# Performance work log

Hardware: AMD Instinct MI355X
Metric: run time of the kernel (lower is better)

## Reference

```python
import jax, jax.numpy as jnp
import numpy as np


def setup_inputs() -> dict:
    key = jax.random.key(0)
    k1, k2, k3 = jax.random.split(key, 3)
    batch, in_features, out_features = 4096, 8192, 8192
    x = jax.random.normal(k1, (batch, in_features), dtype=jnp.float32)
    weight = jax.random.normal(k2, (out_features, in_features), dtype=jnp.float32) * (1.0 / np.sqrt(in_features))
    bias = jax.random.normal(k3, (out_features,), dtype=jnp.float32) * (1.0 / np.sqrt(in_features))
    return {"x": x, "weight": weight, "bias": bias}


def reference(x, weight, bias):
    # Linear: [B, out] = x @ W^T + b
    y = jnp.einsum('bi,oi->bo', x, weight) + bias
    # Per-row sum over out_features, then mean (divide by out_features)
    mean_val = jnp.sum(y, axis=1) / weight.shape[0]  # [B]
    # Two logsumexp ops over a size-1 dim: log(exp(v)) twice == identity,
    # computed explicitly to match the original op chain.
    lse1 = jnp.log(jnp.exp(mean_val))
    lse2 = jnp.log(jnp.exp(lse1))
    return lse2[:, None]  # [B, 1]
```

## Files before the change

### kernel.cpp

```cpp
#include <hip/hip_runtime.h>

typedef float f32x4 __attribute__((ext_vector_type(4)));

constexpr int IN_F  = 8192;
constexpr int OUT_F = 8192;
constexpr int BATCH = 4096;
constexpr int TPB   = 256;
constexpr int S4    = IN_F / 4;

constexpr int CHUNKS = 256;
constexpr int RPC    = OUT_F / CHUNKS;
constexpr int COLG   = IN_F / (TPB * 4);

__global__ __launch_bounds__(TPB) void colsum_kernel(
    const float* __restrict__ W, float* __restrict__ part, int rpc) {
    const int col4 = blockIdx.x * TPB + threadIdx.x;
    const f32x4* __restrict__ p = reinterpret_cast<const f32x4*>(W)
        + (long)blockIdx.y * rpc * S4 + col4;
    f32x4 a0 = {0.f, 0.f, 0.f, 0.f}, a1 = {0.f, 0.f, 0.f, 0.f};
    #pragma unroll 8
    for (int r = 0; r < rpc; r += 2) {
        a0 += p[(long)r * S4];
        a1 += p[(long)(r + 1) * S4];
    }
    reinterpret_cast<f32x4*>(part)[(long)blockIdx.y * S4 + col4] = a0 + a1;
}

__global__ __launch_bounds__(TPB) void combine_kernel(
    const float* __restrict__ part, const float* __restrict__ bias,
    float* __restrict__ wsum, float* __restrict__ bsum) {
    const int blk = blockIdx.x, tid = threadIdx.x;
    if (blk < 256) {
        __shared__ float lds[TPB];
        const int col   = blk * 32 + (tid & 31);
        const int slice = tid >> 5;
        float s = 0.f;
        #pragma unroll 8
        for (int k = 0; k < CHUNKS / 8; ++k)
            s += part[(long)(slice * (CHUNKS / 8) + k) * IN_F + col];
        lds[tid] = s;
        __syncthreads();
        if (tid < 32) {
            float t = 0.f;
            #pragma unroll
            for (int sl = 0; sl < 8; ++sl) t += lds[sl * 32 + tid];
            wsum[blk * 32 + tid] = t;
        }
    } else {
        __shared__ float red[4];
        float bs = 0.f;
        for (int k = tid; k < OUT_F; k += TPB) bs += bias[k];
        #pragma unroll
        for (int o = 32; o; o >>= 1) bs += __shfl_down(bs, o);
        if ((tid & 63) == 0) red[tid >> 6] = bs;
        __syncthreads();
        if (tid == 0) *bsum = red[0] + red[1] + red[2] + red[3];
    }
}

constexpr int NBLK_R = 2048;
constexpr int ROWS_R = BATCH / NBLK_R;

__global__ __launch_bounds__(TPB) void rowdot_kernel(
    const float* __restrict__ x, const float* __restrict__ wsum,
    const float* __restrict__ bsum, float* __restrict__ out) {
    __shared__ float red[8];
    const int tid = threadIdx.x;
    const long rowbase = (long)blockIdx.x * ROWS_R;
    const f32x4* __restrict__ x4 =
        reinterpret_cast<const f32x4*>(x) + rowbase * S4;
    const f32x4* __restrict__ w4 = reinterpret_cast<const f32x4*>(wsum);

    float s0 = 0.f, s1 = 0.f;
    #pragma unroll
    for (int k = tid; k < S4; k += TPB) {
        f32x4 wv = w4[k];
        f32x4 a  = x4[k];
        f32x4 b  = x4[S4 + k];
        s0 += a.x * wv.x + a.y * wv.y + a.z * wv.z + a.w * wv.w;
        s1 += b.x * wv.x + b.y * wv.y + b.z * wv.z + b.w * wv.w;
    }
    #pragma unroll
    for (int o = 32; o; o >>= 1) {
        s0 += __shfl_down(s0, o);
        s1 += __shfl_down(s1, o);
    }
    const int wid = tid >> 6;
    if ((tid & 63) == 0) { red[wid] = s0; red[4 + wid] = s1; }
    __syncthreads();
    if (tid == 0) {
        const float bsv = *bsum;
        out[rowbase]     = (red[0] + red[1] + red[2] + red[3] + bsv) * (1.0f / OUT_F);
        out[rowbase + 1] = (red[4] + red[5] + red[6] + red[7] + bsv) * (1.0f / OUT_F);
    }
}

__global__ __launch_bounds__(TPB) void combine_generic_kernel(
    const float* __restrict__ part, const float* __restrict__ bias,
    float* __restrict__ wsum, float* __restrict__ bsum, int chunks) {
    const int blk = blockIdx.x, tid = threadIdx.x;
    if (blk < 32) {
        const int col = blk * TPB + tid;
        float s = 0.f;
        #pragma unroll 8
        for (int c = 0; c < chunks; ++c) s += part[(long)c * IN_F + col];
        wsum[col] = s;
    } else {
        __shared__ float red[4];
        float bs = 0.f;
        for (int k = tid; k < OUT_F; k += TPB) bs += bias[k];
        #pragma unroll
        for (int o = 32; o; o >>= 1) bs += __shfl_down(bs, o);
        if ((tid & 63) == 0) red[tid >> 6] = bs;
        __syncthreads();
        if (tid == 0) *bsum = red[0] + red[1] + red[2] + red[3];
    }
}

extern "C" void kernel_launch(void* const* d_in, const int* in_sizes, int n_in,
                              void* d_out, int out_size, void* d_ws, size_t ws_size,
                              hipStream_t stream) {
    const float* x    = (const float*)d_in[0];
    const float* W    = (const float*)d_in[1];
    const float* bias = (const float*)d_in[2];
    float*       out  = (float*)d_out;

    if (((size_t)CHUNKS * IN_F + IN_F + 16) * sizeof(float) <= ws_size) {
        float* part = (float*)d_ws;
        float* wsum = part + (size_t)CHUNKS * IN_F;
        float* bsum = wsum + IN_F;
        colsum_kernel<<<dim3(COLG, CHUNKS), TPB, 0, stream>>>(W, part, RPC);
        combine_kernel<<<257, TPB, 0, stream>>>(part, bias, wsum, bsum);
        rowdot_kernel<<<NBLK_R, TPB, 0, stream>>>(x, wsum, bsum, out);
    } else {
        int chunks = 128;
        while (chunks > 1 &&
               ((size_t)chunks * IN_F + IN_F + 16) * sizeof(float) > ws_size)
            chunks >>= 1;
        float* part = (float*)d_ws;
        float* wsum = part + (size_t)chunks * IN_F;
        float* bsum = wsum + IN_F;
        colsum_kernel<<<dim3(COLG, chunks), TPB, 0, stream>>>(W, part, OUT_F / chunks);
        combine_generic_kernel<<<33, TPB, 0, stream>>>(part, bias, wsum, bsum, chunks);
        rowdot_kernel<<<NBLK_R, TPB, 0, stream>>>(x, wsum, bsum, out);
    }
}
```

Baseline: 96.41 us.

## Restructure column-sum into contiguous row chunks and use one-row dot blocks

Replaces the 2D-grid strided column-sum of W with 1024 blocks that each sum 8 contiguous full rows, producing 1024 partial vectors. The combine kernel is reworked for the larger partial count, and the row-dot kernel now handles one batch row per block. The aim is more sequential DRAM access and better latency hiding, at the cost of a larger partial buffer (4x more write and read traffic) and a higher workspace requirement.

After: 95.82 us (median of 2 runs). Within noise of the previous version (-0.6%).

```diff
diff --git a/kernel.cpp b/kernel.cpp
--- a/kernel.cpp
+++ b/kernel.cpp
@@ -8,44 +8,45 @@
 constexpr int TPB   = 256;
 constexpr int S4    = IN_F / 4;
 
-constexpr int CHUNKS = 256;
-constexpr int RPC    = OUT_F / CHUNKS;
-constexpr int COLG   = IN_F / (TPB * 4);
+constexpr int CHUNKS = 1024;
+constexpr int RPCH   = OUT_F / CHUNKS;
+constexpr int CHUNKS_FB = 256;
+constexpr int COLG      = IN_F / (TPB * 4);
 
-__global__ __launch_bounds__(TPB) void colsum_kernel(
-    const float* __restrict__ W, float* __restrict__ part, int rpc) {
-    const int col4 = blockIdx.x * TPB + threadIdx.x;
-    const f32x4* __restrict__ p = reinterpret_cast<const f32x4*>(W)
-        + (long)blockIdx.y * rpc * S4 + col4;
-    f32x4 a0 = {0.f, 0.f, 0.f, 0.f}, a1 = {0.f, 0.f, 0.f, 0.f};
-    #pragma unroll 8
-    for (int r = 0; r < rpc; r += 2) {
-        a0 += p[(long)r * S4];
-        a1 += p[(long)(r + 1) * S4];
+__global__ __launch_bounds__(TPB, 4) void colsum_contig_kernel(
+    const float* __restrict__ W, float* __restrict__ part) {
+    const int tid = threadIdx.x, c = blockIdx.x;
+    const f32x4* __restrict__ p =
+        reinterpret_cast<const f32x4*>(W) + (long)c * RPCH * S4;
+    f32x4 acc[8] = {};
+    #pragma unroll
+    for (int r = 0; r < RPCH; ++r) {
+        #pragma unroll
+        for (int j = 0; j < 8; ++j)
+            acc[j] += p[(long)r * S4 + j * TPB + tid];
     }
-    reinterpret_cast<f32x4*>(part)[(long)blockIdx.y * S4 + col4] = a0 + a1;
+    f32x4* o = reinterpret_cast<f32x4*>(part) + (long)c * S4;
+    #pragma unroll
+    for (int j = 0; j < 8; ++j) o[j * TPB + tid] = acc[j];
 }
 
-__global__ __launch_bounds__(TPB) void combine_kernel(
+__global__ __launch_bounds__(TPB) void combine_c_kernel(
     const float* __restrict__ part, const float* __restrict__ bias,
     float* __restrict__ wsum, float* __restrict__ bsum) {
     const int blk = blockIdx.x, tid = threadIdx.x;
-    if (blk < 256) {
+    if (blk < IN_F / 64) {
         __shared__ float lds[TPB];
-        const int col   = blk * 32 + (tid & 31);
-        const int slice = tid >> 5;
+        const int col = blk * 64 + (tid & 63);
+        const int sl  = tid >> 6;
         float s = 0.f;
         #pragma unroll 8
-        for (int k = 0; k < CHUNKS / 8; ++k)
-            s += part[(long)(slice * (CHUNKS / 8) + k) * IN_F + col];
+        for (int k = 0; k < CHUNKS / 4; ++k)
+            s += part[(long)(sl * (CHUNKS / 4) + k) * IN_F + col];
         lds[tid] = s;
         __syncthreads();
-        if (tid < 32) {
-            float t = 0.f;
-            #pragma unroll
-            for (int sl = 0; sl < 8; ++sl) t += lds[sl * 32 + tid];
-            wsum[blk * 32 + tid] = t;
-        }
+        if (tid < 64)
+            wsum[blk * 64 + tid] =
+                lds[tid] + lds[64 + tid] + lds[128 + tid] + lds[192 + tid];
     } else {
         __shared__ float red[4];
         float bs = 0.f;
@@ -58,44 +59,44 @@
     }
 }
 
-constexpr int NBLK_R = 2048;
-constexpr int ROWS_R = BATCH / NBLK_R;
-
-__global__ __launch_bounds__(TPB) void rowdot_kernel(
+__global__ __launch_bounds__(TPB) void rowdot1_kernel(
     const float* __restrict__ x, const float* __restrict__ wsum,
     const float* __restrict__ bsum, float* __restrict__ out) {
-    __shared__ float red[8];
+    __shared__ float red[4];
     const int tid = threadIdx.x;
-    const long rowbase = (long)blockIdx.x * ROWS_R;
-    const f32x4* __restrict__ x4 =
-        reinterpret_cast<const f32x4*>(x) + rowbase * S4;
+    const long b  = blockIdx.x;
+    const f32x4* __restrict__ x4 = reinterpret_cast<const f32x4*>(x) + b * S4;
     const f32x4* __restrict__ w4 = reinterpret_cast<const f32x4*>(wsum);
-
-    float s0 = 0.f, s1 = 0.f;
+    float s = 0.f;
     #pragma unroll
-    for (int k = tid; k < S4; k += TPB) {
-        f32x4 wv = w4[k];
-        f32x4 a  = x4[k];
-        f32x4 b  = x4[S4 + k];
-        s0 += a.x * wv.x + a.y * wv.y + a.z * wv.z + a.w * wv.w;
-        s1 += b.x * wv.x + b.y * wv.y + b.z * wv.z + b.w * wv.w;
+    for (int j = 0; j < 8; ++j) {
+        f32x4 a = x4[j * TPB + tid];
+        f32x4 w = w4[j * TPB + tid];
+        s += a.x * w.x + a.y * w.y + a.z * w.z + a.w * w.w;
     }
     #pragma unroll
-    for (int o = 32; o; o >>= 1) {
-        s0 += __shfl_down(s0, o);
-        s1 += __shfl_down(s1, o);
-    }
-    const int wid = tid >> 6;
-    if ((tid & 63) == 0) { red[wid] = s0; red[4 + wid] = s1; }
+    for (int o = 32; o; o >>= 1) s += __shfl_down(s, o);
+    if ((tid & 63) == 0) red[tid >> 6] = s;
     __syncthreads();
-    if (tid == 0) {
-        const float bsv = *bsum;
-        out[rowbase]     = (red[0] + red[1] + red[2] + red[3] + bsv) * (1.0f / OUT_F);
-        out[rowbase + 1] = (red[4] + red[5] + red[6] + red[7] + bsv) * (1.0f / OUT_F);
-    }
+    if (tid == 0)
+        out[b] = (red[0] + red[1] + red[2] + red[3] + *bsum) * (1.0f / OUT_F);
 }
 
-__global__ __launch_bounds__(TPB) void combine_generic_kernel(
+__global__ __launch_bounds__(TPB) void colsum_strided_kernel(
+    const float* __restrict__ W, float* __restrict__ part, int rpc) {
+    const int col4 = blockIdx.x * TPB + threadIdx.x;
+    const f32x4* __restrict__ p = reinterpret_cast<const f32x4*>(W)
+        + (long)blockIdx.y * rpc * S4 + col4;
+    f32x4 a0 = {0.f,0.f,0.f,0.f}, a1 = {0.f,0.f,0.f,0.f};
+    #pragma unroll 8
+    for (int r = 0; r < rpc; r += 2) {
+        a0 += p[(long)r * S4];
+        a1 += p[(long)(r + 1) * S4];
+    }
+    reinterpret_cast<f32x4*>(part)[(long)blockIdx.y * S4 + col4] = a0 + a1;
+}
+
+__global__ __launch_bounds__(TPB) void combine_fb_kernel(
     const float* __restrict__ part, const float* __restrict__ bias,
     float* __restrict__ wsum, float* __restrict__ bsum, int chunks) {
     const int blk = blockIdx.x, tid = threadIdx.x;
@@ -129,19 +130,20 @@
         float* part = (float*)d_ws;
         float* wsum = part + (size_t)CHUNKS * IN_F;
         float* bsum = wsum + IN_F;
-        colsum_kernel<<<dim3(COLG, CHUNKS), TPB, 0, stream>>>(W, part, RPC);
-        combine_kernel<<<257, TPB, 0, stream>>>(part, bias, wsum, bsum);
-        rowdot_kernel<<<NBLK_R, TPB, 0, stream>>>(x, wsum, bsum, out);
+        colsum_contig_kernel<<<CHUNKS, TPB, 0, stream>>>(W, part);
+        combine_c_kernel<<<IN_F / 64 + 1, TPB, 0, stream>>>(part, bias, wsum, bsum);
+        rowdot1_kernel<<<BATCH, TPB, 0, stream>>>(x, wsum, bsum, out);
     } else {
-        int chunks = 128;
+        int chunks = CHUNKS_FB;
         while (chunks > 1 &&
                ((size_t)chunks * IN_F + IN_F + 16) * sizeof(float) > ws_size)
             chunks >>= 1;
         float* part = (float*)d_ws;
         float* wsum = part + (size_t)chunks * IN_F;
         float* bsum = wsum + IN_F;
-        colsum_kernel<<<dim3(COLG, chunks), TPB, 0, stream>>>(W, part, OUT_F / chunks);
-        combine_generic_kernel<<<33, TPB, 0, stream>>>(part, bias, wsum, bsum, chunks);
-        rowdot_kernel<<<NBLK_R, TPB, 0, stream>>>(x, wsum, bsum, out);
+        colsum_strided_kernel<<<dim3(COLG, chunks), TPB, 0, stream>>>(
+            W, part, OUT_F / chunks);
+        combine_fb_kernel<<<33, TPB, 0, stream>>>(part, bias, wsum, bsum, chunks);
+        rowdot1_kernel<<<BATCH, TPB, 0, stream>>>(x, wsum, bsum, out);
     }
 }
```

## Fuse colsum, combine and rowdot into one cooperative kernel with grid syncs

Applied to the files above, without the earlier changes.

Replaces the three-kernel pipeline with a single cooperative kernel of 1024 blocks. Each block first computes a partial column sum of W, prefetches two rows of x into registers, then hits a grid sync. After that, 257 blocks combine the partials and the bias, and after a second grid sync every block does a 4-row dot product. This removes two kernel launch boundaries and overlaps x loads with the W reduction, at the cost of grid-wide barriers, high register pressure and host-side occupancy queries on every call.

After: 96.79 us. Within noise of the previous version (+0.4%).

```diff
diff --git a/kernel.cpp b/kernel.cpp
--- a/kernel.cpp
+++ b/kernel.cpp
@@ -1,4 +1,7 @@
 #include <hip/hip_runtime.h>
+#include <hip/hip_cooperative_groups.h>
+
+namespace cg = cooperative_groups;
 
 typedef float f32x4 __attribute__((ext_vector_type(4)));
 
@@ -8,16 +11,120 @@
 constexpr int TPB   = 256;
 constexpr int S4    = IN_F / 4;
 
-constexpr int CHUNKS = 256;
-constexpr int RPC    = OUT_F / CHUNKS;
-constexpr int COLG   = IN_F / (TPB * 4);
-
-__global__ __launch_bounds__(TPB) void colsum_kernel(
+constexpr int NBLK    = 1024;
+constexpr int CHUNKS  = NBLK / 8;
+constexpr int RPC     = OUT_F / CHUNKS;
+constexpr int ROWS    = BATCH / NBLK;
+
+__global__ __launch_bounds__(TPB, 4) void fused2_kernel(
+    const float* __restrict__ x, const float* __restrict__ W,
+    const float* __restrict__ bias, float* __restrict__ out,
+    float* __restrict__ part, float* __restrict__ wsum,
+    float* __restrict__ bsum) {
+
+    __shared__ float lds[TPB];
+    __shared__ float red[16];
+    const int tid = threadIdx.x, blk = blockIdx.x;
+
+    const long rowbase = (long)blk * ROWS;
+    const f32x4* __restrict__ x4 =
+        reinterpret_cast<const f32x4*>(x) + rowbase * S4;
+
+    {
+        const int g = blk & 7, c = blk >> 3;
+        const f32x4* __restrict__ p = reinterpret_cast<const f32x4*>(W)
+            + (long)c * RPC * S4 + g * TPB + tid;
+        f32x4 a0 = {0.f,0.f,0.f,0.f}, a1 = {0.f,0.f,0.f,0.f};
+        #pragma unroll 8
+        for (int r = 0; r < RPC; r += 2) {
+            a0 += p[(long)r * S4];
+            a1 += p[(long)(r + 1) * S4];
+        }
+        reinterpret_cast<f32x4*>(part)[(long)c * S4 + g * TPB + tid] = a0 + a1;
+    }
+
+    f32x4 pf0[8], pf1[8];
+    #pragma unroll
+    for (int j = 0; j < 8; ++j) pf0[j] = x4[j * TPB + tid];
+    #pragma unroll
+    for (int j = 0; j < 8; ++j) pf1[j] = x4[S4 + j * TPB + tid];
+
+    cg::this_grid().sync();
+
+    if (blk < 256) {
+        const int col = blk * 32 + (tid & 31);
+        const int sl  = tid >> 5;
+        float s = 0.f;
+        #pragma unroll
+        for (int k = 0; k < CHUNKS / 8; ++k)
+            s += part[(long)(sl * (CHUNKS / 8) + k) * IN_F + col];
+        lds[tid] = s;
+        __syncthreads();
+        if (tid < 32) {
+            float t = 0.f;
+            #pragma unroll
+            for (int q = 0; q < 8; ++q) t += lds[q * 32 + tid];
+            wsum[blk * 32 + tid] = t;
+        }
+    } else if (blk == 256) {
+        float bs = 0.f;
+        for (int k = tid; k < OUT_F; k += TPB) bs += bias[k];
+        #pragma unroll
+        for (int o = 32; o; o >>= 1) bs += __shfl_down(bs, o);
+        if ((tid & 63) == 0) red[tid >> 6] = bs;
+        __syncthreads();
+        if (tid == 0) *bsum = red[0] + red[1] + red[2] + red[3];
+    }
+
+    cg::this_grid().sync();
+
+    {
+        const f32x4* __restrict__ w4 = reinterpret_cast<const f32x4*>(wsum);
+        float s0 = 0.f, s1 = 0.f, s2 = 0.f, s3 = 0.f;
+        #pragma unroll
+        for (int j = 0; j < 8; ++j) {
+            const int k = j * TPB + tid;
+            f32x4 wv = w4[k];
+            f32x4 a  = pf0[j];
+            f32x4 b  = pf1[j];
+            f32x4 c2 = x4[2 * S4 + k];
+            f32x4 d  = x4[3 * S4 + k];
+            s0 += a.x*wv.x + a.y*wv.y + a.z*wv.z + a.w*wv.w;
+            s1 += b.x*wv.x + b.y*wv.y + b.z*wv.z + b.w*wv.w;
+            s2 += c2.x*wv.x + c2.y*wv.y + c2.z*wv.z + c2.w*wv.w;
+            s3 += d.x*wv.x + d.y*wv.y + d.z*wv.z + d.w*wv.w;
+        }
+        #pragma unroll
+        for (int o = 32; o; o >>= 1) {
+            s0 += __shfl_down(s0, o);
+            s1 += __shfl_down(s1, o);
+            s2 += __shfl_down(s2, o);
+            s3 += __shfl_down(s3, o);
+        }
+        const int wid = tid >> 6;
+        if ((tid & 63) == 0) {
+            red[wid] = s0; red[4 + wid] = s1; red[8 + wid] = s2; red[12 + wid] = s3;
+        }
+        __syncthreads();
+        if (tid == 0) {
+            const float bsv = *bsum;
+            out[rowbase + 0] = (red[0] +red[1] +red[2] +red[3]  + bsv) * (1.0f/OUT_F);
+            out[rowbase + 1] = (red[4] +red[5] +red[6] +red[7]  + bsv) * (1.0f/OUT_F);
+            out[rowbase + 2] = (red[8] +red[9] +red[10]+red[11] + bsv) * (1.0f/OUT_F);
+            out[rowbase + 3] = (red[12]+red[13]+red[14]+red[15] + bsv) * (1.0f/OUT_F);
+        }
+    }
+}
+
+constexpr int CH_FB = 256;
+constexpr int COLG  = IN_F / (TPB * 4);
+
+__global__ __launch_bounds__(TPB) void colsum_fb_kernel(
     const float* __restrict__ W, float* __restrict__ part, int rpc) {
     const int col4 = blockIdx.x * TPB + threadIdx.x;
     const f32x4* __restrict__ p = reinterpret_cast<const f32x4*>(W)
         + (long)blockIdx.y * rpc * S4 + col4;
-    f32x4 a0 = {0.f, 0.f, 0.f, 0.f}, a1 = {0.f, 0.f, 0.f, 0.f};
+    f32x4 a0 = {0.f,0.f,0.f,0.f}, a1 = {0.f,0.f,0.f,0.f};
     #pragma unroll 8
     for (int r = 0; r < rpc; r += 2) {
         a0 += p[(long)r * S4];
@@ -26,24 +133,23 @@
     reinterpret_cast<f32x4*>(part)[(long)blockIdx.y * S4 + col4] = a0 + a1;
 }
 
-__global__ __launch_bounds__(TPB) void combine_kernel(
+__global__ __launch_bounds__(TPB) void combine_fb_kernel(
     const float* __restrict__ part, const float* __restrict__ bias,
-    float* __restrict__ wsum, float* __restrict__ bsum) {
+    float* __restrict__ wsum, float* __restrict__ bsum, int chunks) {
     const int blk = blockIdx.x, tid = threadIdx.x;
     if (blk < 256) {
         __shared__ float lds[TPB];
-        const int col   = blk * 32 + (tid & 31);
-        const int slice = tid >> 5;
+        const int col = blk * 32 + (tid & 31);
+        const int sl  = tid >> 5;
         float s = 0.f;
-        #pragma unroll 8
-        for (int k = 0; k < CHUNKS / 8; ++k)
-            s += part[(long)(slice * (CHUNKS / 8) + k) * IN_F + col];
+        for (int k = 0; k < chunks / 8; ++k)
+            s += part[(long)(sl * (chunks / 8) + k) * IN_F + col];
         lds[tid] = s;
         __syncthreads();
         if (tid < 32) {
             float t = 0.f;
             #pragma unroll
-            for (int sl = 0; sl < 8; ++sl) t += lds[sl * 32 + tid];
+            for (int q = 0; q < 8; ++q) t += lds[q * 32 + tid];
             wsum[blk * 32 + tid] = t;
         }
     } else {
@@ -58,63 +164,27 @@
     }
 }
 
-constexpr int NBLK_R = 2048;
-constexpr int ROWS_R = BATCH / NBLK_R;
-
-__global__ __launch_bounds__(TPB) void rowdot_kernel(
+__global__ __launch_bounds__(TPB) void rowdot_fb_kernel(
     const float* __restrict__ x, const float* __restrict__ wsum,
     const float* __restrict__ bsum, float* __restrict__ out) {
-    __shared__ float red[8];
+    __shared__ float red[4];
     const int tid = threadIdx.x;
-    const long rowbase = (long)blockIdx.x * ROWS_R;
-    const f32x4* __restrict__ x4 =
-        reinterpret_cast<const f32x4*>(x) + rowbase * S4;
+    const long b  = blockIdx.x;
+    const f32x4* __restrict__ x4 = reinterpret_cast<const f32x4*>(x) + b * S4;
     const f32x4* __restrict__ w4 = reinterpret_cast<const f32x4*>(wsum);
-
-    float s0 = 0.f, s1 = 0.f;
-    #pragma unroll
-    for (int k = tid; k < S4; k += TPB) {
-        f32x4 wv = w4[k];
-        f32x4 a  = x4[k];
-        f32x4 b  = x4[S4 + k];
-        s0 += a.x * wv.x + a.y * wv.y + a.z * wv.z + a.w * wv.w;
-        s1 += b.x * wv.x + b.y * wv.y + b.z * wv.z + b.w * wv.w;
-    }
-    #pragma unroll
-    for (int o = 32; o; o >>= 1) {
-        s0 += __shfl_down(s0, o);
-        s1 += __shfl_down(s1, o);
-    }
-    const int wid = tid >> 6;
-    if ((tid & 63) == 0) { red[wid] = s0; red[4 + wid] = s1; }
+    float s = 0.f;
+    #pragma unroll
+    for (int j = 0; j < 8; ++j) {
+        f32x4 a = x4[j * TPB + tid];
+        f32x4 w = w4[j * TPB + tid];
+        s += a.x*w.x + a.y*w.y + a.z*w.z + a.w*w.w;
+    }
+    #pragma unroll
+    for (int o = 32; o; o >>= 1) s += __shfl_down(s, o);
+    if ((tid & 63) == 0) red[tid >> 6] = s;
     __syncthreads();
-    if (tid == 0) {
-        const float bsv = *bsum;
-        out[rowbase]     = (red[0] + red[1] + red[2] + red[3] + bsv) * (1.0f / OUT_F);
-        out[rowbase + 1] = (red[4] + red[5] + red[6] + red[7] + bsv) * (1.0f / OUT_F);
-    }
-}
-
-__global__ __launch_bounds__(TPB) void combine_generic_kernel(
-    const float* __restrict__ part, const float* __restrict__ bias,
-    float* __restrict__ wsum, float* __restrict__ bsum, int chunks) {
-    const int blk = blockIdx.x, tid = threadIdx.x;
-    if (blk < 32) {
-        const int col = blk * TPB + tid;
-        float s = 0.f;
-        #pragma unroll 8
-        for (int c = 0; c < chunks; ++c) s += part[(long)c * IN_F + col];
-        wsum[col] = s;
-    } else {
-        __shared__ float red[4];
-        float bs = 0.f;
-        for (int k = tid; k < OUT_F; k += TPB) bs += bias[k];
-        #pragma unroll
-        for (int o = 32; o; o >>= 1) bs += __shfl_down(bs, o);
-        if ((tid & 63) == 0) red[tid >> 6] = bs;
-        __syncthreads();
-        if (tid == 0) *bsum = red[0] + red[1] + red[2] + red[3];
-    }
+    if (tid == 0)
+        out[b] = (red[0] + red[1] + red[2] + red[3] + *bsum) * (1.0f / OUT_F);
 }
 
 extern "C" void kernel_launch(void* const* d_in, const int* in_sizes, int n_in,
@@ -125,23 +195,32 @@
     const float* bias = (const float*)d_in[2];
     float*       out  = (float*)d_out;
 
-    if (((size_t)CHUNKS * IN_F + IN_F + 16) * sizeof(float) <= ws_size) {
+    int dev = 0;    (void)hipGetDevice(&dev);
+    int coop = 0;   (void)hipDeviceGetAttribute(&coop, hipDeviceAttributeCooperativeLaunch, dev);
+    int ncu = 0;    (void)hipDeviceGetAttribute(&ncu, hipDeviceAttributeMultiprocessorCount, dev);
+    int maxblk = 0;
+    (void)hipOccupancyMaxActiveBlocksPerMultiprocessor(&maxblk, fused2_kernel, TPB, 0);
+
+    const size_t need_c = ((size_t)CHUNKS * IN_F + IN_F + 16) * sizeof(float);
+    if (coop && (long)maxblk * ncu >= NBLK && need_c <= ws_size) {
         float* part = (float*)d_ws;
         float* wsum = part + (size_t)CHUNKS * IN_F;
         float* bsum = wsum + IN_F;
-        colsum_kernel<<<dim3(COLG, CHUNKS), TPB, 0, stream>>>(W, part, RPC);
-        combine_kernel<<<257, TPB, 0, stream>>>(part, bias, wsum, bsum);
-        rowdot_kernel<<<NBLK_R, TPB, 0, stream>>>(x, wsum, bsum, out);
-    } else {
-        int chunks = 128;
-        while (chunks > 1 &&
-               ((size_t)chunks * IN_F + IN_F + 16) * sizeof(float) > ws_size)
-            chunks >>= 1;
-        float* part = (float*)d_ws;
-        float* wsum = part + (size_t)chunks * IN_F;
-        float* bsum = wsum + IN_F;
-        colsum_kernel<<<dim3(COLG, chunks), TPB, 0, stream>>>(W, part, OUT_F / chunks);
-        combine_generic_kernel<<<33, TPB, 0, stream>>>(part, bias, wsum, bsum, chunks);
-        rowdot_kernel<<<NBLK_R, TPB, 0, stream>>>(x, wsum, bsum, out);
-    }
-}
+        void* args[] = {(void*)&x, (void*)&W, (void*)&bias, (void*)&out,
+                        (void*)&part, (void*)&wsum, (void*)&bsum};
+        hipError_t err = hipLaunchCooperativeKernel(
+            (const void*)fused2_kernel, dim3(NBLK), dim3(TPB), args, 0, stream);
+        if (err == hipSuccess) return;
+    }
+
+    int chunks = CH_FB;
+    while (chunks > 8 &&
+           ((size_t)chunks * IN_F + IN_F + 16) * sizeof(float) > ws_size)
+        chunks >>= 1;
+    float* part = (float*)d_ws;
+    float* wsum = part + (size_t)chunks * IN_F;
+    float* bsum = wsum + IN_F;
+    colsum_fb_kernel<<<dim3(COLG, chunks), TPB, 0, stream>>>(W, part, OUT_F / chunks);
+    combine_fb_kernel<<<257, TPB, 0, stream>>>(part, bias, wsum, bsum, chunks);
+    rowdot_fb_kernel<<<BATCH, TPB, 0, stream>>>(x, wsum, bsum, out);
+}
```
